# Kernel optimization log

Measured on AMD Instinct MI355X. Metric: run time of the kernel, lower is better.

## Reference

```python
import jax, jax.numpy as jnp
import numpy as np

N, T_IN, PRE_LEN = 4096, 8, 12
E, H = 64, 128
MAX_NEI_DIS = 5.0


def _lstm_cell(x, h, c, Wih, Whh, bih, bhh):
    # torch.nn.LSTMCell math; gate order i, f, g, o
    gates = x @ Wih.T + bih + h @ Whh.T + bhh
    i, f, g, o = jnp.split(gates, 4, axis=-1)
    i = jax.nn.sigmoid(i)
    f = jax.nn.sigmoid(f)
    g = jnp.tanh(g)
    o = jax.nn.sigmoid(o)
    c_new = f * c + i * g
    return o * jnp.tanh(c_new), c_new


def _social_pool(pos, hidden):
    # sum hidden[j] over j with ||pos_j - pos_i|| < MAX_NEI_DIS (self included)
    d2 = jnp.sum((pos[:, None, :] - pos[None, :, :]) ** 2, axis=-1)  # [N,N]
    mask = (d2 < MAX_NEI_DIS * MAX_NEI_DIS).astype(hidden.dtype)
    return mask @ hidden  # [N,H]


def setup_inputs() -> dict:
    key = jax.random.key(0)
    ks = jax.random.split(key, 10)
    tracks = jax.random.normal(ks[0], (N, T_IN, 2), dtype=jnp.float32) * 20.0
    s = 0.05
    return {
        "tracks": tracks,
        "We": jax.random.normal(ks[1], (E, 2), dtype=jnp.float32) * s,
        "be": jax.random.normal(ks[2], (E,), dtype=jnp.float32) * s,
        "Wih": jax.random.normal(ks[3], (4 * H, H + E), dtype=jnp.float32) * s,
        "Whh": jax.random.normal(ks[4], (4 * H, H), dtype=jnp.float32) * s,
        "bih": jax.random.normal(ks[5], (4 * H,), dtype=jnp.float32) * s,
        "bhh": jax.random.normal(ks[6], (4 * H,), dtype=jnp.float32) * s,
        "Wd": jax.random.normal(ks[7], (2, H), dtype=jnp.float32) * s,
        "bd": jax.random.normal(ks[8], (2,), dtype=jnp.float32) * s,
    }


def reference(tracks, We, be, Wih, Whh, bih, bhh, Wd, bd):
    n = tracks.shape[0]
    emb = lambda p: p @ We.T + be

    # ---- group_encode ----
    x0 = jnp.concatenate([emb(tracks[:, 0]), jnp.zeros((n, H), tracks.dtype)], axis=1)
    h, c = _lstm_cell(x0, jnp.zeros((n, H), tracks.dtype), jnp.zeros((n, H), tracks.dtype),
                      Wih, Whh, bih, bhh)

    def enc_step(carry, pos):
        h, c = carry
        sh = _social_pool(pos, h)
        x = jnp.concatenate([emb(pos), sh], axis=1)
        h, c = _lstm_cell(x, h, c, Wih, Whh, bih, bhh)
        return (h, c), None

    # frame_idx = 0 .. input_len-2 -> positions at frames 0..6
    enc_pos = jnp.swapaxes(tracks[:, : T_IN - 1], 0, 1)  # [7, N, 2]
    (h, c), _ = jax.lax.scan(enc_step, (h, c), enc_pos)

    # ---- decode ----
    def dec_step(carry, _):
        h, c, last = carry
        sh = _social_pool(last, h)
        x = jnp.concatenate([emb(last), sh], axis=1)
        h, c = _lstm_cell(x, h, c, Wih, Whh, bih, bhh)
        delta = h @ Wd.T + bd
        last = last + delta
        return (h, c, last), last[0]

    last = tracks[:, -1]
    _, preds0 = jax.lax.scan(dec_step, (h, c, last), None, length=PRE_LEN)
    # returned group_track[0]: original 8 frames + 12 predicted positions
    return jnp.concatenate([tracks[0], preds0], axis=0)  # [20, 2]
```

## Files before the change

### kernel.cpp

```cpp
#include <hip/hip_runtime.h>
#include <hip/hip_bf16.h>

#define N_AG   4096
#define T_IN   8
#define PRELEN 12
#define EDIM   64
#define HDIM   128
#define KTOT   320
#define GDIM   512
#define KI     10
#define LOSCALE 2048.0f

typedef _Float16 f16x8 __attribute__((ext_vector_type(8)));
typedef _Float16 f16x2 __attribute__((ext_vector_type(2)));
typedef float    f32x4 __attribute__((ext_vector_type(4)));


__global__ __launch_bounds__(256) void init_kernel(
    const float* __restrict__ tracks,
    const float* __restrict__ Wih, const float* __restrict__ Whh,
    const float* __restrict__ bih, const float* __restrict__ bhh,
    float* __restrict__ hA, float* __restrict__ hB, float* __restrict__ c,
    float* __restrict__ lastA, float* __restrict__ lastB,
    _Float16* __restrict__ WfH, _Float16* __restrict__ WfL,
    float* __restrict__ bsum, float* __restrict__ posAll,
    float* __restrict__ h16Af, float* __restrict__ h16Bf,
    float* __restrict__ out)
{
    int idx = blockIdx.x * 256 + threadIdx.x;
    hA[idx] = 0.f;
    hB[idx] = 0.f;
    c[idx]  = 0.f;
    if (idx < 262208) { h16Af[idx] = 0.f; h16Bf[idx] = 0.f; }
    if (idx < KTOT * GDIM) {
        int g = idx / KTOT, k = idx - g * KTOT;
        float val = (k < 192) ? Wih[g * 192 + k] : Whh[g * 128 + (k - 192)];
        int nt = g >> 4, ki = k >> 5;
        int ln = (g & 15) | (((k >> 3) & 3) << 4);
        int e  = k & 7;
        size_t off = (size_t)((nt * KI + ki) * 64 + ln) * 8 + e;
        _Float16 hi = (_Float16)val;
        WfH[off] = hi;
        WfL[off] = (_Float16)((val - (float)hi) * LOSCALE);
    }
    if (idx < N_AG) {
        lastA[idx * 2 + 0] = tracks[idx * 16 + 14];
        lastA[idx * 2 + 1] = tracks[idx * 16 + 15];
        lastB[idx * 2 + 0] = 0.f;
        lastB[idx * 2 + 1] = 0.f;
    }
    if (idx < GDIM) bsum[idx] = bih[idx] + bhh[idx];
    if (idx < 16)  out[idx] = tracks[idx];
    if (idx < 7 * N_AG) {
        int t = idx / N_AG, a = idx & (N_AG - 1);
        posAll[idx * 2 + 0] = tracks[a * 16 + t * 2 + 0];
        posAll[idx * 2 + 1] = tracks[a * 16 + t * 2 + 1];
    }
}

__global__ void __launch_bounds__(1024, 1) social_step(
    const float* __restrict__ pp,
    const float* __restrict__ We, const float* __restrict__ be,
    const _Float16* __restrict__ WfH, const _Float16* __restrict__ WfL,
    const float* __restrict__ bsum,
    const float* __restrict__ hIn, float* __restrict__ hOut,
    const _Float16* __restrict__ h16In, _Float16* __restrict__ h16Out,
    float* __restrict__ c,
    const float* __restrict__ lastIn, float* __restrict__ lastOut,
    const float* __restrict__ Wd, const float* __restrict__ bd,
    float* __restrict__ out,
    int firstStep, int decStep)
{
    __shared__ __align__(16) char smraw[77824];
    _Float16 (*AH)[64][8] = (_Float16(*)[64][8])smraw;
    _Float16 (*AL)[64][8] = (_Float16(*)[64][8])(smraw + 10240);
    float (*shs)[HDIM]    = (float(*)[HDIM])(smraw + 20480);
    unsigned short (*sidx)[512] = (unsigned short(*)[512])(smraw + 28672);
    float (*hs)[HDIM]     = (float(*)[HDIM])(smraw + 28672);
    float* posl           = (float*)(smraw + 45056);
    float* accx           = (float*)(smraw + 45056);

    int tid  = threadIdx.x;
    int lane = tid & 63;
    int wv   = tid >> 6;
    int a0   = blockIdx.x * 16;

    if (!firstStep) {
#pragma unroll
        for (int k = 0; k < 2; k++) {
            int u = tid + k * 1024;
            *(f32x4*)&posl[u * 4] = *(const f32x4*)(pp + (size_t)u * 4);
        }
        __syncthreads();

        const float2* pvl = (const float2*)posl;
        float2 pi = pvl[a0 + wv];
        unsigned long long ltmask = (1ull << lane) - 1ull;
        int cnt = 0;
#pragma unroll 8
        for (int cc = 0; cc < 32; cc++) {
            int j0 = cc * 128 + 2 * lane;
            float4 q4 = *(const float4*)&posl[(size_t)j0 * 2];
            float dx0 = q4.x - pi.x, dy0 = q4.y - pi.y;
            float dx1 = q4.z - pi.x, dy1 = q4.w - pi.y;
            bool p0 = dx0 * dx0 + dy0 * dy0 < 25.0f;
            bool p1 = dx1 * dx1 + dy1 * dy1 < 25.0f;
            unsigned long long m0 = __ballot(p0), m1 = __ballot(p1);
            if (p0) { int s = cnt + __popcll(m0 & ltmask); if (s < 512) sidx[wv][s] = (unsigned short)j0; }
            cnt += __popcll(m0);
            if (p1) { int s = cnt + __popcll(m1 & ltmask); if (s < 512) sidx[wv][s] = (unsigned short)(j0 + 1); }
            cnt += __popcll(m1);
        }
        if (cnt > 512) cnt = 512;
        int cpad = (cnt + 15) & ~15;
        if (cpad > 512) cpad = 512;
        if (lane < cpad - cnt) sidx[wv][cnt + lane] = (unsigned short)N_AG;

        int d0 = lane * 2;
        float s0 = 0.f, s1 = 0.f;
        for (int t2 = 0; t2 < cpad; t2 += 16) {
            f16x2 v[16];
#pragma unroll
            for (int r = 0; r < 16; r++) {
                int j = sidx[wv][t2 + r];
                v[r] = *(const f16x2*)(h16In + (size_t)j * HDIM + d0);
            }
#pragma unroll
            for (int r = 0; r < 16; r++) { s0 += (float)v[r][0]; s1 += (float)v[r][1]; }
        }
        shs[wv][d0]     = s0;
        shs[wv][d0 + 1] = s1;
    }
    __syncthreads();

    for (int u = tid; u < 16 * (KTOT / 8); u += 1024) {
        int a = u & 15, kg = u >> 4;
        int ga = a0 + a;
        int k0 = kg * 8;
        float v[8];
        if (k0 < EDIM) {
            float px = pp[ga * 2], py = pp[ga * 2 + 1];
#pragma unroll
            for (int j = 0; j < 8; j++) {
                int k = k0 + j;
                v[j] = fmaf(px, We[k * 2], fmaf(py, We[k * 2 + 1], be[k]));
            }
        } else if (k0 < EDIM + HDIM) {
#pragma unroll
            for (int j = 0; j < 8; j++)
                v[j] = firstStep ? 0.f : shs[a][k0 - EDIM + j];
        } else {
#pragma unroll
            for (int j = 0; j < 8; j++)
                v[j] = hIn[(unsigned)ga * HDIM + (k0 - EDIM - HDIM + j)];
        }
        f16x8 hi8, lo8;
#pragma unroll
        for (int j = 0; j < 8; j++) {
            _Float16 hv = (_Float16)v[j];
            hi8[j] = hv;
            lo8[j] = (_Float16)((v[j] - (float)hv) * LOSCALE);
        }
        int ki = kg >> 2, ln = a | ((kg & 3) << 4);
        *(f16x8*)&AH[ki][ln][0] = hi8;
        *(f16x8*)&AL[ki][ln][0] = lo8;
    }
    __syncthreads();

    int q    = wv & 7;
    int half = wv >> 3;
    int dcol = q * 16 + (lane & 15);
    const float inv = 1.0f / LOSCALE;

    f32x4 acc[4], accL[4];
#pragma unroll
    for (int g = 0; g < 4; g++) {
        float bb = half ? 0.f : bsum[dcol + g * 128];
        f32x4 z; z[0] = bb; z[1] = bb; z[2] = bb; z[3] = bb;
        acc[g] = z;
        f32x4 zz; zz[0] = 0.f; zz[1] = 0.f; zz[2] = 0.f; zz[3] = 0.f;
        accL[g] = zz;
    }
#pragma unroll
    for (int kk = 0; kk < 5; kk++) {
        int ki = half * 5 + kk;
        f16x8 ah = *(const f16x8*)&AH[ki][lane][0];
        f16x8 al = *(const f16x8*)&AL[ki][lane][0];
#pragma unroll
        for (int g = 0; g < 4; g++) {
            int nt = q + 8 * g;
            size_t off = (size_t)((nt * KI + ki) * 64 + lane) * 8;
            f16x8 bh = *(const f16x8*)&WfH[off];
            f16x8 bl = *(const f16x8*)&WfL[off];
            acc[g]  = __builtin_amdgcn_mfma_f32_16x16x32_f16(ah, bh, acc[g],  0, 0, 0);
            accL[g] = __builtin_amdgcn_mfma_f32_16x16x32_f16(al, bh, accL[g], 0, 0, 0);
            accL[g] = __builtin_amdgcn_mfma_f32_16x16x32_f16(ah, bl, accL[g], 0, 0, 0);
        }
    }
#pragma unroll
    for (int g = 0; g < 4; g++) {
#pragma unroll
        for (int r = 0; r < 4; r++)
            acc[g][r] = fmaf(accL[g][r], inv, acc[g][r]);
    }
    if (half) {
#pragma unroll
        for (int g = 0; g < 4; g++)
            *(f32x4*)&accx[(size_t)((q * 4 + g) * 64 + lane) * 4] = acc[g];
    }
    __syncthreads();

    if (!half) {
#pragma unroll
        for (int g = 0; g < 4; g++) {
            f32x4 o = *(const f32x4*)&accx[(size_t)((q * 4 + g) * 64 + lane) * 4];
#pragma unroll
            for (int r = 0; r < 4; r++) acc[g][r] += o[r];
        }
#pragma unroll
        for (int r = 0; r < 4; r++) {
            int alc = (lane >> 4) * 4 + r;
            int ga  = a0 + alc;
            float vi = acc[0][r], vf = acc[1][r], vg = acc[2][r], vo = acc[3][r];
            float ig = 1.f / (1.f + expf(-vi));
            float fg = 1.f / (1.f + expf(-vf));
            float gg = tanhf(vg);
            float og = 1.f / (1.f + expf(-vo));
            float cold = c[(unsigned)ga * HDIM + dcol];
            float cn = fmaf(fg, cold, ig * gg);
            float hn = og * tanhf(cn);
            c[(unsigned)ga * HDIM + dcol]      = cn;
            hOut[(unsigned)ga * HDIM + dcol]   = hn;
            h16Out[(unsigned)ga * HDIM + dcol] = (_Float16)hn;
            hs[alc][dcol] = hn;
        }
    }

    if (decStep >= 0) {
        __syncthreads();
        if (tid < 512) {
            int ag = tid >> 5, comp = (tid >> 4) & 1, l16 = tid & 15;
            float s = 0.f;
#pragma unroll
            for (int j = 0; j < 8; j++) {
                int d = l16 * 8 + j;
                s += hs[ag][d] * Wd[comp * HDIM + d];
            }
            s += __shfl_down(s, 8, 16);
            s += __shfl_down(s, 4, 16);
            s += __shfl_down(s, 2, 16);
            s += __shfl_down(s, 1, 16);
            if (l16 == 0) {
                int ga = a0 + ag;
                float nl = lastIn[ga * 2 + comp] + s + bd[comp];
                lastOut[ga * 2 + comp] = nl;
                if (ga == 0) out[(8 + decStep) * 2 + comp] = nl;
            }
        }
    }
}

extern "C" void kernel_launch(void* const* d_in, const int* in_sizes, int n_in,
                              void* d_out, int out_size, void* d_ws, size_t ws_size,
                              hipStream_t stream)
{
    const float* tracks = (const float*)d_in[0];
    const float* We     = (const float*)d_in[1];
    const float* be     = (const float*)d_in[2];
    const float* Wih    = (const float*)d_in[3];
    const float* Whh    = (const float*)d_in[4];
    const float* bih    = (const float*)d_in[5];
    const float* bhh    = (const float*)d_in[6];
    const float* Wd     = (const float*)d_in[7];
    const float* bd     = (const float*)d_in[8];
    float* out = (float*)d_out;
    float* ws  = (float*)d_ws;

    float*     hA     = ws;
    float*     hB     = ws + 524288;
    float*     c      = ws + 1048576;
    float*     lastA  = ws + 1572864;
    float*     lastB  = ws + 1581056;
    float*     bsum   = ws + 1589248;
    float*     posAll = ws + 1589760;
    _Float16*  WfH    = (_Float16*)(ws + 1647104);
    _Float16*  WfL    = (_Float16*)(ws + 1729024);
    float*     h16Af  = ws + 1810944;
    float*     h16Bf  = ws + 2073152;

    float*    hbuf[2]   = { hA, hB };
    _Float16* h16buf[2] = { (_Float16*)h16Af, (_Float16*)h16Bf };
    float*    lbuf[2]   = { lastA, lastB };

    init_kernel<<<2048, 256, 0, stream>>>(tracks, Wih, Whh, bih, bhh,
                                          hA, hB, c, lastA, lastB,
                                          WfH, WfL, bsum, posAll,
                                          h16Af, h16Bf, out);

    int k = 0;
    auto step = [&](const float* pp, const float* lin, float* lout,
                    int fs, int ds) {
        social_step<<<256, 1024, 0, stream>>>(
            pp, We, be, WfH, WfL, bsum,
            hbuf[(k + 1) & 1], hbuf[k & 1],
            h16buf[(k + 1) & 1], h16buf[k & 1],
            c, lin, lout, Wd, bd, out, fs, ds);
        k++;
    };

    step(posAll, nullptr, nullptr, 1, -1);

    for (int t = 0; t < T_IN - 1; t++)
        step(posAll + (size_t)t * N_AG * 2, nullptr, nullptr, 0, -1);

    for (int s = 0; s < PRELEN; s++)
        step(lbuf[s & 1], lbuf[s & 1], lbuf[(s + 1) & 1], 0, s);
}
```

Measured before the change: 446.1 us.

## Split neighbor search across waves with ballot masks and widen gather loads

The neighbor search is restructured. Each wave now tests a 256-candidate slice against all 16 block agents, writes 64-bit ballot masks to shared memory, and each wave then compacts its agent's mask into an index list with shuffles. Before, each wave scanned all 4096 positions for a single agent. The hidden-state gather now loads f16x4 per lane with two rows per pass and a cross-half shuffle reduction, and the embedding/h parts of the A-tile are packed before the search so that work overlaps. In exchange it uses more shared memory and adds an extra barrier.

Result: slower. 557.0 us (+24.9%).

```diff
diff --git a/kernel.cpp b/kernel.cpp
--- a/kernel.cpp
+++ b/kernel.cpp
@@ -12,7 +12,7 @@
 #define LOSCALE 2048.0f
 
 typedef _Float16 f16x8 __attribute__((ext_vector_type(8)));
-typedef _Float16 f16x2 __attribute__((ext_vector_type(2)));
+typedef _Float16 f16x4 __attribute__((ext_vector_type(4)));
 typedef float    f32x4 __attribute__((ext_vector_type(4)));
 
 
@@ -71,7 +71,7 @@
     float* __restrict__ out,
     int firstStep, int decStep)
 {
-    __shared__ __align__(16) char smraw[77824];
+    __shared__ __align__(16) char smraw[86272];
     _Float16 (*AH)[64][8] = (_Float16(*)[64][8])smraw;
     _Float16 (*AL)[64][8] = (_Float16(*)[64][8])(smraw + 10240);
     float (*shs)[HDIM]    = (float(*)[HDIM])(smraw + 20480);
@@ -79,6 +79,7 @@
     float (*hs)[HDIM]     = (float(*)[HDIM])(smraw + 28672);
     float* posl           = (float*)(smraw + 45056);
     float* accx           = (float*)(smraw + 45056);
+    unsigned long long* masksL = (unsigned long long*)(smraw + 77824);
 
     int tid  = threadIdx.x;
     int lane = tid & 63;
@@ -91,50 +92,11 @@
             int u = tid + k * 1024;
             *(f32x4*)&posl[u * 4] = *(const f32x4*)(pp + (size_t)u * 4);
         }
-        __syncthreads();
-
-        const float2* pvl = (const float2*)posl;
-        float2 pi = pvl[a0 + wv];
-        unsigned long long ltmask = (1ull << lane) - 1ull;
-        int cnt = 0;
-#pragma unroll 8
-        for (int cc = 0; cc < 32; cc++) {
-            int j0 = cc * 128 + 2 * lane;
-            float4 q4 = *(const float4*)&posl[(size_t)j0 * 2];
-            float dx0 = q4.x - pi.x, dy0 = q4.y - pi.y;
-            float dx1 = q4.z - pi.x, dy1 = q4.w - pi.y;
-            bool p0 = dx0 * dx0 + dy0 * dy0 < 25.0f;
-            bool p1 = dx1 * dx1 + dy1 * dy1 < 25.0f;
-            unsigned long long m0 = __ballot(p0), m1 = __ballot(p1);
-            if (p0) { int s = cnt + __popcll(m0 & ltmask); if (s < 512) sidx[wv][s] = (unsigned short)j0; }
-            cnt += __popcll(m0);
-            if (p1) { int s = cnt + __popcll(m1 & ltmask); if (s < 512) sidx[wv][s] = (unsigned short)(j0 + 1); }
-            cnt += __popcll(m1);
-        }
-        if (cnt > 512) cnt = 512;
-        int cpad = (cnt + 15) & ~15;
-        if (cpad > 512) cpad = 512;
-        if (lane < cpad - cnt) sidx[wv][cnt + lane] = (unsigned short)N_AG;
-
-        int d0 = lane * 2;
-        float s0 = 0.f, s1 = 0.f;
-        for (int t2 = 0; t2 < cpad; t2 += 16) {
-            f16x2 v[16];
-#pragma unroll
-            for (int r = 0; r < 16; r++) {
-                int j = sidx[wv][t2 + r];
-                v[r] = *(const f16x2*)(h16In + (size_t)j * HDIM + d0);
-            }
-#pragma unroll
-            for (int r = 0; r < 16; r++) { s0 += (float)v[r][0]; s1 += (float)v[r][1]; }
-        }
-        shs[wv][d0]     = s0;
-        shs[wv][d0 + 1] = s1;
-    }
-    __syncthreads();
-
-    for (int u = tid; u < 16 * (KTOT / 8); u += 1024) {
-        int a = u & 15, kg = u >> 4;
+    }
+
+    for (int u = tid; u < 16 * 24; u += 1024) {
+        int a = u & 15, v_ = u >> 4;
+        int kg = (v_ < 8) ? v_ : v_ + 16;
         int ga = a0 + a;
         int k0 = kg * 8;
         float v[8];
@@ -145,15 +107,93 @@
                 int k = k0 + j;
                 v[j] = fmaf(px, We[k * 2], fmaf(py, We[k * 2 + 1], be[k]));
             }
-        } else if (k0 < EDIM + HDIM) {
-#pragma unroll
-            for (int j = 0; j < 8; j++)
-                v[j] = firstStep ? 0.f : shs[a][k0 - EDIM + j];
         } else {
 #pragma unroll
             for (int j = 0; j < 8; j++)
                 v[j] = hIn[(unsigned)ga * HDIM + (k0 - EDIM - HDIM + j)];
         }
+        f16x8 hi8, lo8;
+#pragma unroll
+        for (int j = 0; j < 8; j++) {
+            _Float16 hv = (_Float16)v[j];
+            hi8[j] = hv;
+            lo8[j] = (_Float16)((v[j] - (float)hv) * LOSCALE);
+        }
+        int ki = kg >> 2, ln = a | ((kg & 3) << 4);
+        *(f16x8*)&AH[ki][ln][0] = hi8;
+        *(f16x8*)&AL[ki][ln][0] = lo8;
+    }
+    __syncthreads();
+
+    if (!firstStep) {
+        const float2* pvl = (const float2*)posl;
+#pragma unroll
+        for (int s = 0; s < 4; s++) {
+            int cand = wv * 256 + s * 64 + lane;
+            float2 pj = pvl[cand];
+            unsigned long long mkw = 0;
+#pragma unroll
+            for (int a = 0; a < 16; a++) {
+                float2 pa = pvl[a0 + a];
+                float dx = pj.x - pa.x, dy = pj.y - pa.y;
+                unsigned long long m = __ballot(dx * dx + dy * dy < 25.0f);
+                if (lane == a) mkw = m;
+            }
+            if (lane < 16) masksL[lane * 66 + wv * 4 + s] = mkw;
+        }
+        __syncthreads();
+
+        unsigned long long myw = masksL[wv * 66 + lane];
+        unsigned long long ltmask = (1ull << lane) - 1ull;
+        int cnt = 0;
+#pragma unroll 8
+        for (int k = 0; k < 64; k++) {
+            unsigned long long wk = __shfl(myw, k);
+            if ((wk >> lane) & 1ull) {
+                int s = cnt + __popcll(wk & ltmask);
+                if (s < 512) sidx[wv][s] = (unsigned short)(k * 64 + lane);
+            }
+            cnt += __popcll(wk);
+        }
+        if (cnt > 512) cnt = 512;
+        int cpad = (cnt + 31) & ~31;
+        if (cpad > 512) cpad = 512;
+        if (lane < cpad - cnt) sidx[wv][cnt + lane] = (unsigned short)N_AG;
+
+        int rhalf = lane >> 5;
+        int dq    = (lane & 31) * 4;
+        float s0 = 0.f, s1 = 0.f, s2 = 0.f, s3 = 0.f;
+        for (int t2 = 0; t2 < cpad; t2 += 32) {
+            f16x4 v[16];
+#pragma unroll
+            for (int u = 0; u < 16; u++) {
+                int j = sidx[wv][t2 + 2 * u + rhalf];
+                v[u] = *(const f16x4*)(h16In + (size_t)j * HDIM + dq);
+            }
+#pragma unroll
+            for (int u = 0; u < 16; u++) {
+                s0 += (float)v[u][0]; s1 += (float)v[u][1];
+                s2 += (float)v[u][2]; s3 += (float)v[u][3];
+            }
+        }
+        s0 += __shfl_xor(s0, 32);
+        s1 += __shfl_xor(s1, 32);
+        s2 += __shfl_xor(s2, 32);
+        s3 += __shfl_xor(s3, 32);
+        if (rhalf == 0) {
+            f32x4 r; r[0] = s0; r[1] = s1; r[2] = s2; r[3] = s3;
+            *(f32x4*)&shs[wv][dq] = r;
+        }
+    }
+    __syncthreads();
+
+    for (int u = tid; u < 16 * 16; u += 1024) {
+        int a = u & 15, kg = 8 + (u >> 4);
+        int k0 = kg * 8;
+        float v[8];
+#pragma unroll
+        for (int j = 0; j < 8; j++)
+            v[j] = firstStep ? 0.f : shs[a][k0 - EDIM + j];
         f16x8 hi8, lo8;
 #pragma unroll
         for (int j = 0; j < 8; j++) {
```
